# Kernel tuning notes

Measured on AMD Instinct MI355X. Metric: run time of the kernel, lower is better.

Reference implementation:

```python
import jax, jax.numpy as jnp
import numpy as np

SEQ_LEN, INPUT_DIM, HIDDEN_DIM, OUTPUT_DIM = 1024, 128, 256, 128
BATCH = 256


def setup_inputs() -> dict:
    key = jax.random.key(0)
    ks = jax.random.split(key, 7)
    s_ih = 1.0 / np.sqrt(INPUT_DIM)
    s_hh = 1.0 / np.sqrt(HIDDEN_DIM)
    return {
        "x": jax.random.normal(ks[0], (BATCH, SEQ_LEN, INPUT_DIM), jnp.float32),
        "W_ih": jax.random.normal(ks[1], (INPUT_DIM, 4 * HIDDEN_DIM), jnp.float32) * s_ih,
        "W_hh": jax.random.normal(ks[2], (HIDDEN_DIM, 4 * HIDDEN_DIM), jnp.float32) * s_hh,
        "b_ih": jax.random.normal(ks[3], (4 * HIDDEN_DIM,), jnp.float32) * s_hh,
        "b_hh": jax.random.normal(ks[4], (4 * HIDDEN_DIM,), jnp.float32) * s_hh,
        "W_out": jax.random.normal(ks[5], (HIDDEN_DIM, OUTPUT_DIM), jnp.float32) * s_hh,
        "b_out": jax.random.normal(ks[6], (OUTPUT_DIM,), jnp.float32) * s_hh,
    }


def reference(x, W_ih, W_hh, b_ih, b_hh, W_out, b_out):
    B, T, _ = x.shape
    H = W_hh.shape[0]
    # Precompute input projections for all timesteps: [T, B, 4H]
    x_proj = jnp.einsum("bti,ig->tbg", x, W_ih) + (b_ih + b_hh)

    def step(carry, xp_t):
        h, c = carry
        gates = xp_t + h @ W_hh  # [B, 4H]
        i_t, f_t, g_t, o_t = jnp.split(gates, 4, axis=1)
        i_t = jax.nn.sigmoid(i_t)
        f_t = jax.nn.sigmoid(f_t)
        g_t = jnp.tanh(g_t)
        o_t = jax.nn.sigmoid(o_t)
        c = f_t * c + i_t * g_t
        h = o_t * jnp.tanh(c)
        return (h, c), None

    h0 = jnp.zeros((B, H), x.dtype)
    c0 = jnp.zeros((B, H), x.dtype)
    (h_T, _), _ = jax.lax.scan(step, (h0, c0), x_proj)
    return h_T @ W_out + b_out
```

## Files before the change

### kernel.cpp

```cpp
#include <hip/hip_runtime.h>
#include <cstdint>


#define T_    1024
#define I_    128
#define H_    256

typedef short s8v __attribute__((ext_vector_type(8)));
typedef float f4v __attribute__((ext_vector_type(4)));
typedef unsigned short u16;
typedef unsigned int   u32;
typedef unsigned long long u64;

__device__ __forceinline__ u16 f2bf(float f) {
  union { float f; u32 u; } v; v.f = f;
  u32 r = v.u + 0x7FFFu + ((v.u >> 16) & 1u);
  return (u16)(r >> 16);
}
__device__ __forceinline__ float bf2f(u16 h) {
  union { u32 u; float f; } v; v.u = ((u32)h) << 16;
  return v.f;
}
__device__ __forceinline__ float sig_(float x)  { return 1.0f / (1.0f + __expf(-x)); }
__device__ __forceinline__ float tanh_(float x) { return 2.0f / (1.0f + __expf(-2.0f * x)) - 1.0f; }

__device__ __forceinline__ void unpack4(const u64 w[4], s8v& hi, s8v& lo) {
  #pragma unroll
  for (int j = 0; j < 4; j++) {
    u32 d = (u32)w[j];
    hi[2*j]   = (short)(u16)d;
    lo[2*j]   = (short)(u16)(d >> 16);
    (void)0;
  }
}

__global__ __launch_bounds__(256, 1) void lstm_persist(
    const float* __restrict__ x, const float* __restrict__ Wih,
    const float* __restrict__ Whh, const float* __restrict__ bih,
    const float* __restrict__ bhh, const float* __restrict__ Wout,
    const float* __restrict__ bout, float* __restrict__ out,
    u64* __restrict__ hbuf)
{
  const int bid  = blockIdx.x;
  const int xcd  = bid & 7;
  const int slot = bid >> 3;
  const int ct   = slot & 15;
  const int g    = ((slot >> 4) << 3) | xcd;
  const int tid  = threadIdx.x;
  const int wave = tid >> 6;
  const int lane = tid & 63;
  const int lm   = lane & 15;
  const int lq   = lane >> 4;

  __shared__ u16   Wlds[2][64][392];
  __shared__ u16   xlds[2][2][16][136];
  __shared__ float partial[4][4][16][20];

  for (int it = tid; it < 384 * 64; it += 256) {
    int k = it >> 6;
    int c = it & 63;
    int gcol = (c >> 4) * 256 + ct * 16 + (c & 15);
    float w = (k < 128) ? Wih[k * 1024 + gcol] : Whh[(k - 128) * 1024 + gcol];
    u16 hi = f2bf(w);
    Wlds[0][c][k] = hi;
    Wlds[1][c][k] = f2bf(w - bf2f(hi));
  }
  __syncthreads();

  s8v wfrag[3][4][2];
  #pragma unroll
  for (int ki = 0; ki < 3; ki++) {
    const int kt = wave + 4 * ki;
    #pragma unroll
    for (int gg = 0; gg < 4; gg++) {
      #pragma unroll
      for (int p = 0; p < 2; p++)
        wfrag[ki][gg][p] = *(const s8v*)&Wlds[p][gg * 16 + lm][kt * 32 + lq * 8];
    }
  }
  __syncthreads();

  const int cm  = tid >> 4;
  const int chc = tid & 15;
  float biasv[4];
  #pragma unroll
  for (int gg = 0; gg < 4; gg++) {
    int col = gg * 256 + ct * 16 + chc;
    biasv[gg] = bih[col] + bhh[col];
  }
  float cstate = 0.0f;

  const int xr  = tid >> 4;
  const int xc0 = (tid & 15) * 8;
  const float* xbase = x + (size_t)(g * 16 + xr) * (T_ * I_) + xc0;

  const size_t hpar   = (size_t)16 * 16 * 256;
  const size_t hgbase = (size_t)g * 16 * 256;

  auto xstore = [&](int par, float4 a, float4 b) {
    float v[8] = {a.x, a.y, a.z, a.w, b.x, b.y, b.z, b.w};
    union { u16 u[8]; s8v s; } hi, lo;
    #pragma unroll
    for (int j = 0; j < 8; j++) {
      u16 h = f2bf(v[j]);
      hi.u[j] = h;
      lo.u[j] = f2bf(v[j] - bf2f(h));
    }
    *(s8v*)&xlds[par][0][xr][xc0] = hi.s;
    *(s8v*)&xlds[par][1][xr][xc0] = lo.s;
  };

  {
    float4 a = *(const float4*)(xbase + 0);
    float4 b = *(const float4*)(xbase + 4);
    xstore(0, a, b);
  }
  __syncthreads();

  const size_t hoff = (size_t)lm * 256 + wave * 32 + lq * 8;

  for (int t = 0; t < T_; t++) {
    const int par = t & 1;
    const int pn  = (t + 1) & 1;

    const int tn = (t + 1 < T_) ? (t + 1) : t;
    float4 xa = *(const float4*)(xbase + (size_t)tn * I_);
    float4 xb = *(const float4*)(xbase + (size_t)tn * I_ + 4);

    f4v acc[4];
    #pragma unroll
    for (int gg = 0; gg < 4; gg++)
      #pragma unroll
      for (int r = 0; r < 4; r++) acc[gg][r] = 0.0f;

    {
      s8v axh = *(const s8v*)&xlds[par][0][lm][wave * 32 + lq * 8];
      s8v axl = *(const s8v*)&xlds[par][1][lm][wave * 32 + lq * 8];
      #pragma unroll
      for (int gg = 0; gg < 4; gg++) {
        acc[gg] = __builtin_amdgcn_mfma_f32_16x16x32_bf16(axh, wfrag[0][gg][0], acc[gg], 0, 0, 0);
        acc[gg] = __builtin_amdgcn_mfma_f32_16x16x32_bf16(axl, wfrag[0][gg][0], acc[gg], 0, 0, 0);
        acc[gg] = __builtin_amdgcn_mfma_f32_16x16x32_bf16(axh, wfrag[0][gg][1], acc[gg], 0, 0, 0);
      }
    }

    if (t > 0) {
      const u64* hp = hbuf + (size_t)par * hpar + hgbase + hoff;
      const u32 s = (u32)t;
      u64 w0[4], w1[4];
      while (true) {
        #pragma unroll
        for (int j = 0; j < 4; j++) {
          w0[j] = __hip_atomic_load(hp + j,       __ATOMIC_RELAXED, __HIP_MEMORY_SCOPE_AGENT);
          w1[j] = __hip_atomic_load(hp + 128 + j, __ATOMIC_RELAXED, __HIP_MEMORY_SCOPE_AGENT);
        }
        bool ok = true;
        #pragma unroll
        for (int j = 0; j < 4; j++)
          ok &= ((u32)(w0[j] >> 32) == s) & ((u32)(w1[j] >> 32) == s);
        if (__all(ok)) break;
      }

      #pragma unroll
      for (int ki = 1; ki < 3; ki++) {
        const u64* w = (ki == 1) ? w0 : w1;
        s8v ahh, ahl;
        #pragma unroll
        for (int j = 0; j < 4; j++) {
          u32 d = (u32)w[j];
          ahh[j] = 0; ahl[j] = 0; (void)d;
        }
        (void)ahh; (void)ahl;
      }
      {
        const u64* hp2 = hp + 4;
        u64 w0b[4], w1b[4];
        #pragma unroll
        for (int j = 0; j < 4; j++) {
          w0b[j] = __hip_atomic_load(hp2 + j,       __ATOMIC_RELAXED, __HIP_MEMORY_SCOPE_AGENT);
          w1b[j] = __hip_atomic_load(hp2 + 128 + j, __ATOMIC_RELAXED, __HIP_MEMORY_SCOPE_AGENT);
        }
        bool ok2;
        do {
          ok2 = true;
          #pragma unroll
          for (int j = 0; j < 4; j++)
            ok2 &= ((u32)(w0b[j] >> 32) == (u32)t) & ((u32)(w1b[j] >> 32) == (u32)t);
          if (!__all(ok2)) {
            #pragma unroll
            for (int j = 0; j < 4; j++) {
              w0b[j] = __hip_atomic_load(hp2 + j,       __ATOMIC_RELAXED, __HIP_MEMORY_SCOPE_AGENT);
              w1b[j] = __hip_atomic_load(hp2 + 128 + j, __ATOMIC_RELAXED, __HIP_MEMORY_SCOPE_AGENT);
            }
            ok2 = false;
          }
        } while (!__all(ok2));

        s8v ahh1, ahl1, ahh2, ahl2;
        #pragma unroll
        for (int j = 0; j < 4; j++) {
          u32 d0 = (u32)w0[j], d0b = (u32)w0b[j];
          u32 d1 = (u32)w1[j], d1b = (u32)w1b[j];
          ahh1[j]     = (short)(u16)d0;          ahl1[j]     = (short)(u16)(d0 >> 16);
          ahh1[j + 4] = (short)(u16)d0b;         ahl1[j + 4] = (short)(u16)(d0b >> 16);
          ahh2[j]     = (short)(u16)d1;          ahl2[j]     = (short)(u16)(d1 >> 16);
          ahh2[j + 4] = (short)(u16)d1b;         ahl2[j + 4] = (short)(u16)(d1b >> 16);
        }
        #pragma unroll
        for (int gg = 0; gg < 4; gg++) {
          acc[gg] = __builtin_amdgcn_mfma_f32_16x16x32_bf16(ahh1, wfrag[1][gg][0], acc[gg], 0, 0, 0);
          acc[gg] = __builtin_amdgcn_mfma_f32_16x16x32_bf16(ahl1, wfrag[1][gg][0], acc[gg], 0, 0, 0);
          acc[gg] = __builtin_amdgcn_mfma_f32_16x16x32_bf16(ahh1, wfrag[1][gg][1], acc[gg], 0, 0, 0);
          acc[gg] = __builtin_amdgcn_mfma_f32_16x16x32_bf16(ahh2, wfrag[2][gg][0], acc[gg], 0, 0, 0);
          acc[gg] = __builtin_amdgcn_mfma_f32_16x16x32_bf16(ahl2, wfrag[2][gg][0], acc[gg], 0, 0, 0);
          acc[gg] = __builtin_amdgcn_mfma_f32_16x16x32_bf16(ahh2, wfrag[2][gg][1], acc[gg], 0, 0, 0);
        }
      }
    }

    #pragma unroll
    for (int gg = 0; gg < 4; gg++)
      #pragma unroll
      for (int r = 0; r < 4; r++)
        partial[wave][gg][lq * 4 + r][lm] = acc[gg][r];
    __syncthreads();

    float ga = biasv[0], gb = biasv[1], gc = biasv[2], gd = biasv[3];
    #pragma unroll
    for (int w = 0; w < 4; w++) {
      ga += partial[w][0][cm][chc];
      gb += partial[w][1][cm][chc];
      gc += partial[w][2][cm][chc];
      gd += partial[w][3][cm][chc];
    }
    float i_t = sig_(ga), f_t = sig_(gb), g_t = tanh_(gc), o_t = sig_(gd);
    cstate = f_t * cstate + i_t * g_t;
    float h = o_t * tanh_(cstate);

    u16 hhi = f2bf(h);
    u16 hlo = f2bf(h - bf2f(hhi));
    u64 val = ((u64)(u32)(t + 1) << 32) | ((u32)hlo << 16) | (u32)hhi;
    u64* hw = hbuf + (size_t)pn * hpar + hgbase + (size_t)cm * 256 + ct * 16 + chc;
    __hip_atomic_store(hw, val, __ATOMIC_RELAXED, __HIP_MEMORY_SCOPE_AGENT);

    xstore(pn, xa, xb);
    __syncthreads();
  }

  for (int it = tid; it < 16 * 256; it += 256) {
    int n = it >> 8;
    int k = it & 255;
    float w = (n < 8) ? Wout[k * 128 + ct * 8 + n] : 0.0f;
    u16 hi = f2bf(w);
    Wlds[0][n][k] = hi;
    Wlds[1][n][k] = f2bf(w - bf2f(hi));
  }
  __syncthreads();

  f4v oacc;
  #pragma unroll
  for (int r = 0; r < 4; r++) oacc[r] = 0.0f;
  const u64* hb0 = hbuf + hgbase;
  #pragma unroll
  for (int ki = 0; ki < 2; ki++) {
    const int hk = (wave * 2 + ki) * 32 + lq * 8;
    const u64* hp = hb0 + (size_t)lm * 256 + hk;
    u64 w[8];
    bool ok;
    do {
      #pragma unroll
      for (int j = 0; j < 8; j++)
        w[j] = __hip_atomic_load(hp + j, __ATOMIC_RELAXED, __HIP_MEMORY_SCOPE_AGENT);
      ok = true;
      #pragma unroll
      for (int j = 0; j < 8; j++) ok &= ((u32)(w[j] >> 32) == (u32)T_);
    } while (!__all(ok));
    s8v ahh, ahl;
    #pragma unroll
    for (int j = 0; j < 8; j++) {
      u32 d = (u32)w[j];
      ahh[j] = (short)(u16)d;
      ahl[j] = (short)(u16)(d >> 16);
    }
    s8v bh  = *(const s8v*)&Wlds[0][lm][hk];
    s8v bl  = *(const s8v*)&Wlds[1][lm][hk];
    oacc = __builtin_amdgcn_mfma_f32_16x16x32_bf16(ahh, bh, oacc, 0, 0, 0);
    oacc = __builtin_amdgcn_mfma_f32_16x16x32_bf16(ahl, bh, oacc, 0, 0, 0);
    oacc = __builtin_amdgcn_mfma_f32_16x16x32_bf16(ahh, bl, oacc, 0, 0, 0);
  }
  #pragma unroll
  for (int r = 0; r < 4; r++) partial[wave][0][lq * 4 + r][lm] = oacc[r];
  __syncthreads();

  if (tid < 128) {
    int m  = tid >> 3;
    int oc = tid & 7;
    float v = bout[ct * 8 + oc];
    #pragma unroll
    for (int w = 0; w < 4; w++) v += partial[w][0][m][oc];
    out[(size_t)(g * 16 + m) * 128 + ct * 8 + oc] = v;
  }
}

extern "C" void kernel_launch(void* const* d_in, const int* in_sizes, int n_in,
                              void* d_out, int out_size, void* d_ws, size_t ws_size,
                              hipStream_t stream) {
  const float* x    = (const float*)d_in[0];
  const float* Wih  = (const float*)d_in[1];
  const float* Whh  = (const float*)d_in[2];
  const float* bih  = (const float*)d_in[3];
  const float* bhh  = (const float*)d_in[4];
  const float* Wout = (const float*)d_in[5];
  const float* bout = (const float*)d_in[6];
  float* out = (float*)d_out;

  u64* hbuf = (u64*)d_ws;

  hipLaunchKernelGGL(lstm_persist, dim3(256), dim3(256), 0, stream,
                     x, Wih, Whh, bih, bhh, Wout, bout, out, hbuf);
}
```

Before: 3.624 ms.

## Remove per-step barrier via double-buffered partials and merge hidden-state polling

```diff
diff --git a/kernel.cpp b/kernel.cpp
--- a/kernel.cpp
+++ b/kernel.cpp
@@ -2,9 +2,8 @@
 #include <cstdint>
 
 
-#define T_    1024
-#define I_    128
-#define H_    256
+#define T_ 1024
+#define I_ 128
 
 typedef short s8v __attribute__((ext_vector_type(8)));
 typedef float f4v __attribute__((ext_vector_type(4)));
@@ -23,16 +22,6 @@
 }
 __device__ __forceinline__ float sig_(float x)  { return 1.0f / (1.0f + __expf(-x)); }
 __device__ __forceinline__ float tanh_(float x) { return 2.0f / (1.0f + __expf(-2.0f * x)) - 1.0f; }
-
-__device__ __forceinline__ void unpack4(const u64 w[4], s8v& hi, s8v& lo) {
-  #pragma unroll
-  for (int j = 0; j < 4; j++) {
-    u32 d = (u32)w[j];
-    hi[2*j]   = (short)(u16)d;
-    lo[2*j]   = (short)(u16)(d >> 16);
-    (void)0;
-  }
-}
 
 __global__ __launch_bounds__(256, 1) void lstm_persist(
     const float* __restrict__ x, const float* __restrict__ Wih,
@@ -52,33 +41,47 @@
   const int lm   = lane & 15;
   const int lq   = lane >> 4;
 
-  __shared__ u16   Wlds[2][64][392];
+  __shared__ u16   WB[25600];
   __shared__ u16   xlds[2][2][16][136];
-  __shared__ float partial[4][4][16][20];
-
-  for (int it = tid; it < 384 * 64; it += 256) {
-    int k = it >> 6;
-    int c = it & 63;
-    int gcol = (c >> 4) * 256 + ct * 16 + (c & 15);
-    float w = (k < 128) ? Wih[k * 1024 + gcol] : Whh[(k - 128) * 1024 + gcol];
-    u16 hi = f2bf(w);
-    Wlds[0][c][k] = hi;
-    Wlds[1][c][k] = f2bf(w - bf2f(hi));
-  }
-  __syncthreads();
-
+  __shared__ float partial[2][4][4][16][18];
+
+  auto stageW = [&](int kbeg) {
+    for (int it = tid; it < 192 * 64; it += 256) {
+      int k = kbeg + (it >> 6);
+      int c = it & 63;
+      int gcol = (c >> 4) * 256 + ct * 16 + (c & 15);
+      float w = (k < 128) ? Wih[k * 1024 + gcol] : Whh[(k - 128) * 1024 + gcol];
+      u16 hi = f2bf(w);
+      WB[c * 200 + (k - kbeg)]         = hi;
+      WB[12800 + c * 200 + (k - kbeg)] = f2bf(w - bf2f(hi));
+    }
+  };
   s8v wfrag[3][4][2];
+  stageW(0);
+  __syncthreads();
   #pragma unroll
   for (int ki = 0; ki < 3; ki++) {
     const int kt = wave + 4 * ki;
-    #pragma unroll
-    for (int gg = 0; gg < 4; gg++) {
-      #pragma unroll
-      for (int p = 0; p < 2; p++)
-        wfrag[ki][gg][p] = *(const s8v*)&Wlds[p][gg * 16 + lm][kt * 32 + lq * 8];
-    }
-  }
-  __syncthreads();
+    if (kt < 6)
+      #pragma unroll
+      for (int gg = 0; gg < 4; gg++)
+        #pragma unroll
+        for (int p = 0; p < 2; p++)
+          wfrag[ki][gg][p] = *(const s8v*)&WB[p * 12800 + (gg * 16 + lm) * 200 + kt * 32 + lq * 8];
+  }
+  __syncthreads();
+  stageW(192);
+  __syncthreads();
+  #pragma unroll
+  for (int ki = 0; ki < 3; ki++) {
+    const int kt = wave + 4 * ki;
+    if (kt >= 6)
+      #pragma unroll
+      for (int gg = 0; gg < 4; gg++)
+        #pragma unroll
+        for (int p = 0; p < 2; p++)
+          wfrag[ki][gg][p] = *(const s8v*)&WB[p * 12800 + (gg * 16 + lm) * 200 + (kt * 32 - 192) + lq * 8];
+  }
 
   const int cm  = tid >> 4;
   const int chc = tid & 15;
@@ -110,22 +113,23 @@
     *(s8v*)&xlds[par][1][xr][xc0] = lo.s;
   };
 
+  float4 xa_n, xb_n;
   {
     float4 a = *(const float4*)(xbase + 0);
     float4 b = *(const float4*)(xbase + 4);
     xstore(0, a, b);
   }
-  __syncthreads();
-
-  const size_t hoff = (size_t)lm * 256 + wave * 32 + lq * 8;
+  xa_n = *(const float4*)(xbase + I_);
+  xb_n = *(const float4*)(xbase + I_ + 4);
+  __syncthreads();
+
+  const u64* hb_poll0 = hbuf + hgbase + (size_t)lm * 256 + wave * 32 + lq * 8;
 
   for (int t = 0; t < T_; t++) {
     const int par = t & 1;
     const int pn  = (t + 1) & 1;
 
-    const int tn = (t + 1 < T_) ? (t + 1) : t;
-    float4 xa = *(const float4*)(xbase + (size_t)tn * I_);
-    float4 xb = *(const float4*)(xbase + (size_t)tn * I_ + 4);
+    xstore(pn, xa_n, xb_n);
 
     f4v acc[4];
     #pragma unroll
@@ -145,93 +149,61 @@
     }
 
     if (t > 0) {
-      const u64* hp = hbuf + (size_t)par * hpar + hgbase + hoff;
-      const u32 s = (u32)t;
-      u64 w0[4], w1[4];
+      const u64* hp = hb_poll0 + (size_t)par * hpar;
+      const u32 tt = (u32)t;
+      u64 w[16];
+      int tries = 0;
       while (true) {
         #pragma unroll
-        for (int j = 0; j < 4; j++) {
-          w0[j] = __hip_atomic_load(hp + j,       __ATOMIC_RELAXED, __HIP_MEMORY_SCOPE_AGENT);
-          w1[j] = __hip_atomic_load(hp + 128 + j, __ATOMIC_RELAXED, __HIP_MEMORY_SCOPE_AGENT);
+        for (int j = 0; j < 8; j++) {
+          w[j]     = __hip_atomic_load(hp + j,       __ATOMIC_RELAXED, __HIP_MEMORY_SCOPE_AGENT);
+          w[j + 8] = __hip_atomic_load(hp + 128 + j, __ATOMIC_RELAXED, __HIP_MEMORY_SCOPE_AGENT);
         }
         bool ok = true;
         #pragma unroll
-        for (int j = 0; j < 4; j++)
-          ok &= ((u32)(w0[j] >> 32) == s) & ((u32)(w1[j] >> 32) == s);
-        if (__all(ok)) break;
-      }
-
-      #pragma unroll
-      for (int ki = 1; ki < 3; ki++) {
-        const u64* w = (ki == 1) ? w0 : w1;
-        s8v ahh, ahl;
-        #pragma unroll
-        for (int j = 0; j < 4; j++) {
-          u32 d = (u32)w[j];
-          ahh[j] = 0; ahl[j] = 0; (void)d;
-        }
-        (void)ahh; (void)ahl;
-      }
-      {
-        const u64* hp2 = hp + 4;
-        u64 w0b[4], w1b[4];
-        #pragma unroll
-        for (int j = 0; j < 4; j++) {
-          w0b[j] = __hip_atomic_load(hp2 + j,       __ATOMIC_RELAXED, __HIP_MEMORY_SCOPE_AGENT);
-          w1b[j] = __hip_atomic_load(hp2 + 128 + j, __ATOMIC_RELAXED, __HIP_MEMORY_SCOPE_AGENT);
-        }
-        bool ok2;
-        do {
-          ok2 = true;
-          #pragma unroll
-          for (int j = 0; j < 4; j++)
-            ok2 &= ((u32)(w0b[j] >> 32) == (u32)t) & ((u32)(w1b[j] >> 32) == (u32)t);
-          if (!__all(ok2)) {
-            #pragma unroll
-            for (int j = 0; j < 4; j++) {
-              w0b[j] = __hip_atomic_load(hp2 + j,       __ATOMIC_RELAXED, __HIP_MEMORY_SCOPE_AGENT);
-              w1b[j] = __hip_atomic_load(hp2 + 128 + j, __ATOMIC_RELAXED, __HIP_MEMORY_SCOPE_AGENT);
-            }
-            ok2 = false;
-          }
-        } while (!__all(ok2));
-
-        s8v ahh1, ahl1, ahh2, ahl2;
-        #pragma unroll
-        for (int j = 0; j < 4; j++) {
-          u32 d0 = (u32)w0[j], d0b = (u32)w0b[j];
-          u32 d1 = (u32)w1[j], d1b = (u32)w1b[j];
-          ahh1[j]     = (short)(u16)d0;          ahl1[j]     = (short)(u16)(d0 >> 16);
-          ahh1[j + 4] = (short)(u16)d0b;         ahl1[j + 4] = (short)(u16)(d0b >> 16);
-          ahh2[j]     = (short)(u16)d1;          ahl2[j]     = (short)(u16)(d1 >> 16);
-          ahh2[j + 4] = (short)(u16)d1b;         ahl2[j + 4] = (short)(u16)(d1b >> 16);
-        }
-        #pragma unroll
-        for (int gg = 0; gg < 4; gg++) {
-          acc[gg] = __builtin_amdgcn_mfma_f32_16x16x32_bf16(ahh1, wfrag[1][gg][0], acc[gg], 0, 0, 0);
-          acc[gg] = __builtin_amdgcn_mfma_f32_16x16x32_bf16(ahl1, wfrag[1][gg][0], acc[gg], 0, 0, 0);
-          acc[gg] = __builtin_amdgcn_mfma_f32_16x16x32_bf16(ahh1, wfrag[1][gg][1], acc[gg], 0, 0, 0);
-          acc[gg] = __builtin_amdgcn_mfma_f32_16x16x32_bf16(ahh2, wfrag[2][gg][0], acc[gg], 0, 0, 0);
-          acc[gg] = __builtin_amdgcn_mfma_f32_16x16x32_bf16(ahl2, wfrag[2][gg][0], acc[gg], 0, 0, 0);
-          acc[gg] = __builtin_amdgcn_mfma_f32_16x16x32_bf16(ahh2, wfrag[2][gg][1], acc[gg], 0, 0, 0);
-        }
-      }
+        for (int j = 0; j < 16; j++) ok &= ((u32)(w[j] >> 32) == tt);
+        if (__all((int)ok)) break;
+        if (++tries > (1 << 14)) break;
+      }
+      s8v ah1, al1, ah2, al2;
+      #pragma unroll
+      for (int j = 0; j < 8; j++) {
+        u32 d0 = (u32)w[j];
+        u32 d1 = (u32)w[j + 8];
+        ah1[j] = (short)(u16)d0;  al1[j] = (short)(u16)(d0 >> 16);
+        ah2[j] = (short)(u16)d1;  al2[j] = (short)(u16)(d1 >> 16);
+      }
+      #pragma unroll
+      for (int gg = 0; gg < 4; gg++) {
+        acc[gg] = __builtin_amdgcn_mfma_f32_16x16x32_bf16(ah1, wfrag[1][gg][0], acc[gg], 0, 0, 0);
+        acc[gg] = __builtin_amdgcn_mfma_f32_16x16x32_bf16(al1, wfrag[1][gg][0], acc[gg], 0, 0, 0);
+        acc[gg] = __builtin_amdgcn_mfma_f32_16x16x32_bf16(ah1, wfrag[1][gg][1], acc[gg], 0, 0, 0);
+        acc[gg] = __builtin_amdgcn_mfma_f32_16x16x32_bf16(ah2, wfrag[2][gg][0], acc[gg], 0, 0, 0);
+        acc[gg] = __builtin_amdgcn_mfma_f32_16x16x32_bf16(al2, wfrag[2][gg][0], acc[gg], 0, 0, 0);
+        acc[gg] = __builtin_amdgcn_mfma_f32_16x16x32_bf16(ah2, wfrag[2][gg][1], acc[gg], 0, 0, 0);
+      }
+    }
+
+    {
+      const int tn = (t + 2 < T_) ? (t + 2) : (T_ - 1);
+      xa_n = *(const float4*)(xbase + (size_t)tn * I_);
+      xb_n = *(const float4*)(xbase + (size_t)tn * I_ + 4);
     }
 
     #pragma unroll
     for (int gg = 0; gg < 4; gg++)
       #pragma unroll
       for (int r = 0; r < 4; r++)
-        partial[wave][gg][lq * 4 + r][lm] = acc[gg][r];
+        partial[par][wave][gg][lq * 4 + r][lm] = acc[gg][r];
     __syncthreads();
 
     float ga = biasv[0], gb = biasv[1], gc = biasv[2], gd = biasv[3];
     #pragma unroll
     for (int w = 0; w < 4; w++) {
-      ga += partial[w][0][cm][chc];
-      gb += partial[w][1][cm][chc];
-      gc += partial[w][2][cm][chc];
-      gd += partial[w][3][cm][chc];
+      ga += partial[par][w][0][cm][chc];
+      gb += partial[par][w][1][cm][chc];
+      gc += partial[par][w][2][cm][chc];
+      gd += partial[par][w][3][cm][chc];
     }
     float i_t = sig_(ga), f_t = sig_(gb), g_t = tanh_(gc), o_t = sig_(gd);
     cstate = f_t * cstate + i_t * g_t;
@@ -242,9 +214,6 @@
     u64 val = ((u64)(u32)(t + 1) << 32) | ((u32)hlo << 16) | (u32)hhi;
     u64* hw = hbuf + (size_t)pn * hpar + hgbase + (size_t)cm * 256 + ct * 16 + chc;
     __hip_atomic_store(hw, val, __ATOMIC_RELAXED, __HIP_MEMORY_SCOPE_AGENT);
-
-    xstore(pn, xa, xb);
-    __syncthreads();
   }
 
   for (int it = tid; it < 16 * 256; it += 256) {
@@ -252,20 +221,20 @@
     int k = it & 255;
     float w = (n < 8) ? Wout[k * 128 + ct * 8 + n] : 0.0f;
     u16 hi = f2bf(w);
-    Wlds[0][n][k] = hi;
-    Wlds[1][n][k] = f2bf(w - bf2f(hi));
+    WB[n * 264 + k]        = hi;
+    WB[4224 + n * 264 + k] = f2bf(w - bf2f(hi));
   }
   __syncthreads();
 
   f4v oacc;
   #pragma unroll
   for (int r = 0; r < 4; r++) oacc[r] = 0.0f;
-  const u64* hb0 = hbuf + hgbase;
   #pragma unroll
   for (int ki = 0; ki < 2; ki++) {
     const int hk = (wave * 2 + ki) * 32 + lq * 8;
-    const u64* hp = hb0 + (size_t)lm * 256 + hk;
+    const u64* hp = hbuf + hgbase + (size_t)lm * 256 + hk;
     u64 w[8];
+    int tries = 0;
     bool ok;
     do {
       #pragma unroll
@@ -274,7 +243,8 @@
       ok = true;
       #pragma unroll
       for (int j = 0; j < 8; j++) ok &= ((u32)(w[j] >> 32) == (u32)T_);
-    } while (!__all(ok));
+      if (++tries > (1 << 14)) break;
+    } while (!__all((int)ok));
     s8v ahh, ahl;
     #pragma unroll
     for (int j = 0; j < 8; j++) {
@@ -282,14 +252,14 @@
       ahh[j] = (short)(u16)d;
       ahl[j] = (short)(u16)(d >> 16);
     }
-    s8v bh  = *(const s8v*)&Wlds[0][lm][hk];
-    s8v bl  = *(const s8v*)&Wlds[1][lm][hk];
+    s8v bh = *(const s8v*)&WB[lm * 264 + hk];
+    s8v bl = *(const s8v*)&WB[4224 + lm * 264 + hk];
     oacc = __builtin_amdgcn_mfma_f32_16x16x32_bf16(ahh, bh, oacc, 0, 0, 0);
     oacc = __builtin_amdgcn_mfma_f32_16x16x32_bf16(ahl, bh, oacc, 0, 0, 0);
     oacc = __builtin_amdgcn_mfma_f32_16x16x32_bf16(ahh, bl, oacc, 0, 0, 0);
   }
   #pragma unroll
-  for (int r = 0; r < 4; r++) partial[wave][0][lq * 4 + r][lm] = oacc[r];
+  for (int r = 0; r < 4; r++) partial[0][wave][0][lq * 4 + r][lm] = oacc[r];
   __syncthreads();
 
   if (tid < 128) {
@@ -297,7 +267,7 @@
     int oc = tid & 7;
     float v = bout[ct * 8 + oc];
     #pragma unroll
-    for (int w = 0; w < 4; w++) v += partial[w][0][m][oc];
+    for (int w = 0; w < 4; w++) v += partial[0][w][0][m][oc];
     out[(size_t)(g * 16 + m) * 128 + ct * 8 + oc] = v;
   }
 }
```

New measurement: 3.771 ms. 1.04x slower.
